# Kernel optimization log

Hardware: AMD Instinct MI355X
Metric: run time of the kernel (lower is better)

Reference implementation:

```python
import jax, jax.numpy as jnp
import numpy as np

N, E, P = 50000, 800000, 100000
IN, HID, H, L = 128, 128, 8, 3
D = HID // H


def setup_inputs() -> dict:
    key = jax.random.key(0)
    ks = jax.random.split(key, 24)
    rn = lambda k, shape, s: (jax.random.normal(k, shape, jnp.float32) * s)
    inp = {
        'x': jax.random.normal(ks[0], (N, IN), jnp.float32),
        'edge_src': jax.random.randint(ks[1], (E,), 0, N, jnp.int32),
        'edge_dst': jax.random.randint(ks[2], (E,), 0, N, jnp.int32),
        'edge_w': jax.random.uniform(ks[3], (E,), jnp.float32),
        'pos_src': jax.random.randint(ks[4], (P,), 0, N, jnp.int32),
        'pos_dst': jax.random.randint(ks[5], (P,), 0, N, jnp.int32),
        'neg_src': jax.random.randint(ks[6], (P,), 0, N, jnp.int32),
        'neg_dst': jax.random.randint(ks[7], (P,), 0, N, jnp.int32),
        # input projection
        'W_in': rn(ks[8], (IN, HID), IN ** -0.5),
        'b_in': jnp.zeros((HID,), jnp.float32),
        # per-layer HGT params (single ntype/etype -> plain matrices)
        'Wk': rn(ks[9], (L, HID, HID), HID ** -0.5),
        'Wq': rn(ks[10], (L, HID, HID), HID ** -0.5),
        'Wv': rn(ks[11], (L, HID, HID), HID ** -0.5),
        'att_w': rn(ks[12], (L, H, D, D), D ** -0.5),
        'msg_w': rn(ks[13], (L, H, D, D), D ** -0.5),
        'pri': jnp.ones((L, H), jnp.float32),
        'Wa': rn(ks[14], (L, HID, HID), HID ** -0.5),
        'skip': jnp.ones((L,), jnp.float32),
        # predictor MLP
        'W1': rn(ks[15], (HID, HID // 2), HID ** -0.5),
        'b1': jnp.zeros((HID // 2,), jnp.float32),
        'W2': rn(ks[16], (HID // 2, HID // 4), (HID // 2) ** -0.5),
        'b2': jnp.zeros((HID // 4,), jnp.float32),
        'W3': rn(ks[17], (HID // 4, 1), (HID // 4) ** -0.5),
        'b3': jnp.zeros((1,), jnp.float32),
    }
    return inp


def _hgt_forward(x, edge_src, edge_dst, edge_w, pos_src, pos_dst, neg_src, neg_dst,
                 W_in, b_in, Wk, Wq, Wv, att_w, msg_w, pri, Wa, skip,
                 W1, b1, W2, b2, W3, b3):
    n = x.shape[0]
    nheads = att_w.shape[1]
    d = att_w.shape[2]
    sqrt_d = jnp.asarray(d ** 0.5, x.dtype)
    h = jax.nn.relu(x @ W_in + b_in)
    nlayers = Wk.shape[0]
    for l in range(nlayers):
        k = (h @ Wk[l]).reshape(n, nheads, d)
        q = (h @ Wq[l]).reshape(n, nheads, d)
        v = (h @ Wv[l]).reshape(n, nheads, d)
        # relation-specific per-head transforms (etype constant -> node-level)
        kw = jnp.einsum('nhd,hde->nhe', k, att_w[l])
        mv = jnp.einsum('nhd,hde->nhe', v, msg_w[l])
        # per-edge attention logits [E, H]
        a = (kw[edge_src] * q[edge_dst]).sum(-1) * pri[l] / sqrt_d
        # edge softmax grouped by destination node
        amax = jax.ops.segment_max(a, edge_dst, num_segments=n)[edge_dst]
        ex = jnp.exp(a - amax)
        denom = jax.ops.segment_sum(ex, edge_dst, num_segments=n)[edge_dst]
        attn = ex / denom
        # weighted messages + scatter-sum  [E,H,D] -> [N,H,D]
        m = mv[edge_src] * edge_w[:, None, None] * attn[:, :, None]
        agg = jax.ops.segment_sum(m, edge_dst, num_segments=n).reshape(n, nheads * d)
        hn = agg @ Wa[l]  # linear_a (dropout is identity in eval)
        alpha = jax.nn.sigmoid(skip[l])
        h = hn * alpha + h * (1.0 - alpha)
        if l != nlayers - 1:
            h = jax.nn.relu(h)  # inter-layer relu (dropout identity)
    def predictor(z):
        z = jax.nn.leaky_relu(z @ W1 + b1, 0.2)
        z = jax.nn.leaky_relu(z @ W2 + b2, 0.2)
        return z @ W3 + b3
    h_pos = predictor(h[pos_src] * h[pos_dst])
    h_neg = predictor(h[neg_src] * h[neg_dst])
    return h_pos, h_neg, h


def reference(x, edge_src, edge_dst, edge_w, pos_src, pos_dst, neg_src, neg_dst,
              W_in, b_in, Wk, Wq, Wv, att_w, msg_w, pri, Wa, skip,
              W1, b1, W2, b2, W3, b3):
    return _hgt_forward(x, edge_src, edge_dst, edge_w, pos_src, pos_dst,
                        neg_src, neg_dst, W_in, b_in, Wk, Wq, Wv, att_w,
                        msg_w, pri, Wa, skip, W1, b1, W2, b2, W3, b3)
```

## Files before the change

kernel.cpp:

```cpp
#include <hip/hip_runtime.h>
#include <cstddef>

#define N_NODES 50000
#define N_EDGES 800000
#define N_PAIRS 100000

typedef float floatx4 __attribute__((ext_vector_type(4)));
typedef _Float16 half2v __attribute__((ext_vector_type(2)));
typedef _Float16 half4v __attribute__((ext_vector_type(4)));
typedef _Float16 half8v __attribute__((ext_vector_type(8)));

#define LWAIT { asm volatile("s_waitcnt lgkmcnt(0)" ::: "memory"); __builtin_amdgcn_sched_barrier(0); }

__device__ inline size_t packA(int m, int k, int K) {
  return ((size_t)((m >> 4) * (K >> 5) + (k >> 5)) << 9) +
         ((((unsigned)k >> 3) & 3) << 7) + ((m & 15) << 3) + (k & 7);
}

__device__ inline float fold_val(int l, int r, int j, const float* Wk, const float* Wq,
                                 const float* Wv, const float* att, const float* msg,
                                 const float* pri) {
  if (j >= 128 && j < 256) return Wq[(l * 128 + r) * 128 + (j - 128)];
  int jj = j & 127, hh = jj >> 4, e = jj & 15;
  const float* W = (j < 128) ? Wk : Wv;
  const float* T = (j < 128) ? att : msg;
  float s = 0.f;
#pragma unroll
  for (int d = 0; d < 16; d++)
    s += W[(l * 128 + r) * 128 + hh * 16 + d] * T[((l * 8 + hh) * 16 + d) * 16 + e];
  if (j < 128) s *= pri[l * 8 + hh] * 0.25f;
  return s;
}

__global__ void prep_fused(const float* __restrict__ W_in, const float* __restrict__ Wk,
                           const float* __restrict__ Wq, const float* __restrict__ Wv,
                           const float* __restrict__ att, const float* __restrict__ msg,
                           const float* __restrict__ pri, const float* __restrict__ Wa,
                           const float* __restrict__ W1, const float* __restrict__ W2,
                           _Float16* Wint, _Float16* Wcat, _Float16* Waf,
                           _Float16* W1f, _Float16* W2f,
                           const int* __restrict__ dst, int* __restrict__ deg, int E) {
  if (blockIdx.x >= 880) {
    int g = (blockIdx.x - 880) * 256 + threadIdx.x;
    if (g < E) atomicAdd(&deg[dst[g]], 1);
    return;
  }
  int gid = blockIdx.x * 256 + threadIdx.x;
  float v;
  _Float16* dt;
  size_t o;
  if (gid < 16384) {
    int n = gid >> 7, k = gid & 127;
    v = W_in[k * 128 + n];
    dt = Wint; o = packA(n, k, 128);
  } else if (gid < 163840) {
    int t = gid - 16384;
    int l = t / 49152, u = t - l * 49152;
    int n = u >> 7, k = u & 127;
    v = fold_val(l, k, n, Wk, Wq, Wv, att, msg, pri);
    dt = Wcat + (size_t)l * 49152;
    o = packA(n, k, 128);
  } else if (gid < 212992) {
    int t = gid - 163840;
    int l = t / 16384, u = t & 16383;
    int n = u >> 7, k = u & 127;
    v = Wa[(size_t)l * 16384 + k * 128 + n];
    dt = Waf + (size_t)l * 16384;
    o = packA(n, k, 128);
  } else if (gid < 221184) {
    int u = gid - 212992;
    int n = u >> 7, k = u & 127;
    v = W1[k * 64 + n];
    dt = W1f; o = packA(n, k, 128);
  } else if (gid < 225280) {
    int u = gid - 221184;
    int n = u >> 6, k = u & 63;
    v = (n < 32) ? W2[k * 32 + n] : 0.f;
    dt = W2f; o = packA(n, k, 64);
  } else {
    return;
  }
  dt[o] = (_Float16)v;
}

__global__ void scanA_kernel(const int* __restrict__ deg, int* __restrict__ offs,
                             int* __restrict__ bsum, int* __restrict__ bh, int n) {
  __shared__ int sm[256];
  __shared__ int lh[256];
  int t = threadIdx.x;
  int i = blockIdx.x * 256 + t;
  int dv = (i < n) ? deg[i] : 0;
  int v = (i < n) ? ((dv + 7) & ~7) : 0;
  sm[t] = v;
  __syncthreads();
  for (int off = 1; off < 256; off <<= 1) {
    int u = (t >= off) ? sm[t - off] : 0;
    __syncthreads();
    sm[t] += u;
    __syncthreads();
  }
  if (i < n) offs[i] = sm[t] - v;
  if (t == 255) bsum[blockIdx.x] = sm[255];
  lh[t] = 0;
  __syncthreads();
  if (i < n) atomicAdd(&lh[min(dv, 255)], 1);
  __syncthreads();
  if (lh[t]) atomicAdd(&bh[t], lh[t]);
}

__global__ void scanC_fused(int* __restrict__ offs, const int* __restrict__ bsum,
                            const int* __restrict__ bh, int* __restrict__ balloc,
                            const int* __restrict__ deg, int* __restrict__ cursor,
                            int* __restrict__ perm, int nb, int n) {
  __shared__ int sA[256], sB[256], bcurL[256], lh[256], lbase[256];
  int t = threadIdx.x;
  int i = blockIdx.x * 256 + t;
  int vA = (t < nb) ? bsum[t] : 0;
  sA[t] = vA;
  __syncthreads();
  for (int off = 1; off < 256; off <<= 1) {
    int u = (t >= off) ? sA[t - off] : 0;
    __syncthreads();
    sA[t] += u;
    __syncthreads();
  }
  int boffx = sA[blockIdx.x] - bsum[blockIdx.x];
  int vB = bh[255 - t];
  sB[t] = vB;
  __syncthreads();
  for (int off = 1; off < 256; off <<= 1) {
    int u = (t >= off) ? sB[t - off] : 0;
    __syncthreads();
    sB[t] += u;
    __syncthreads();
  }
  bcurL[255 - t] = sB[t] - vB;
  __syncthreads();
  int o = 0, dv = 0;
  if (i < n) {
    o = offs[i] + boffx;
    offs[i] = o;
    cursor[i] = o;
    dv = deg[i];
  }
  if (blockIdx.x == nb - 1 && t == nb - 1) offs[n] = sA[nb - 1];
  lh[t] = 0;
  __syncthreads();
  int b = 0, local = 0;
  if (i < n) {
    b = min(dv, 255);
    local = atomicAdd(&lh[b], 1);
  }
  __syncthreads();
  int cnt = lh[t];
  lbase[t] = cnt ? atomicAdd(&balloc[t], cnt) : 0;
  __syncthreads();
  if (i < n) perm[bcurL[b] + lbase[b] + local] = i;
}

__global__ void scatter_kernel(const int* __restrict__ src, const int* __restrict__ dst,
                               const float* __restrict__ w, int* __restrict__ cursor,
                               int2* __restrict__ eld, int E) {
  int g = blockIdx.x * blockDim.x + threadIdx.x;
  if (g < E) {
    int d = dst[g];
    int p = atomicAdd(&cursor[d], 1);
    eld[p] = make_int2(src[g], __float_as_int(w[g]));
  }
}

template <int FIRST>
__global__ __launch_bounds__(256) void fused_layer(
    const float* __restrict__ x, const _Float16* __restrict__ aggp,
    const _Float16* __restrict__ Wg1, const float* __restrict__ bias,
    const float* __restrict__ skipv, _Float16* __restrict__ hbuf,
    const _Float16* __restrict__ Wcat_l,
    _Float16* __restrict__ kwmv, _Float16* __restrict__ qbuf, int M) {
  int tid = threadIdx.x;
  int wave = tid >> 6, lane = tid & 63;
  int l16 = lane & 15, q = lane >> 4;
  int g = q, mloc = l16;
  int t0 = (blockIdx.x * 4 + wave) * 2;

  __shared__ _Float16 htile_s[4][2][2048];
  __shared__ float ldsT_s[4][16 * 68];
  float* myT = ldsT_s[wave];

  float alpha = 1.f, beta = 0.f;
  if (!FIRST) {
    float sv = *skipv;
    alpha = 1.f / (1.f + __expf(-sv));
    beta = 1.f - alpha;
  }

  floatx4 acc[2][8];
#pragma unroll
  for (int t = 0; t < 2; t++)
#pragma unroll
    for (int nt = 0; nt < 8; nt++) acc[t][nt] = (floatx4){0.f, 0.f, 0.f, 0.f};

#pragma unroll
  for (int kc = 0; kc < 4; kc++) {
    half8v a0, a1;
#pragma unroll
    for (int t = 0; t < 2; t++) {
      int tile = t0 + t;
      int tileC = (tile * 16 < M) ? tile : 0;
      half8v av;
      if (FIRST) {
        int row = min(tile * 16 + l16, M - 1);
        const float* p = x + (size_t)row * 128 + kc * 32 + q * 8;
        float4 u0 = *(const float4*)p, u1 = *(const float4*)(p + 4);
        float f[8] = {u0.x, u0.y, u0.z, u0.w, u1.x, u1.y, u1.z, u1.w};
#pragma unroll
        for (int i = 0; i < 8; i++) av[i] = (_Float16)f[i];
      } else {
        av = *(const half8v*)(aggp + (size_t)tileC * 2048 + (kc << 9) + lane * 8);
      }
      if (t == 0) a0 = av; else a1 = av;
    }
#pragma unroll
    for (int nt = 0; nt < 8; nt++) {
      half8v b = *(const half8v*)(Wg1 + (size_t)nt * 2048 + (kc << 9) + lane * 8);
      acc[0][nt] = __builtin_amdgcn_mfma_f32_16x16x32_f16(a0, b, acc[0][nt], 0, 0, 0);
      acc[1][nt] = __builtin_amdgcn_mfma_f32_16x16x32_f16(a1, b, acc[1][nt], 0, 0, 0);
    }
  }

#pragma unroll
  for (int t = 0; t < 2; t++) {
    int tile = t0 + t;
    bool alive = tile * 16 < M;
    int tileC = alive ? tile : 0;
#pragma unroll
    for (int p = 0; p < 2; p++) {
#pragma unroll
      for (int ntl = 0; ntl < 4; ntl++)
#pragma unroll
        for (int r = 0; r < 4; r++)
          myT[(q * 4 + r) * 68 + ntl * 16 + l16] = acc[t][p * 4 + ntl][r];
      LWAIT;
#pragma unroll
      for (int kc2 = 0; kc2 < 2; kc2++) {
        const float* rp = myT + mloc * 68 + kc2 * 32 + g * 8;
        floatx4 v0 = *(const floatx4*)rp;
        floatx4 v1 = *(const floatx4*)(rp + 4);
        float vals[8] = {v0[0], v0[1], v0[2], v0[3], v1[0], v1[1], v1[2], v1[3]};
        int col0 = p * 64 + kc2 * 32 + g * 8;
        size_t pbaseL = ((size_t)(tileC * 4 + (col0 >> 5)) << 9) + (size_t)lane * 8;
        if (FIRST) {
          float4 bb0 = *(const float4*)&bias[col0];
          float4 bb1 = *(const float4*)&bias[col0 + 4];
          float bbv[8] = {bb0.x, bb0.y, bb0.z, bb0.w, bb1.x, bb1.y, bb1.z, bb1.w};
#pragma unroll
          for (int j = 0; j < 8; j++) vals[j] = fmaxf(vals[j] + bbv[j], 0.f);
        } else {
          half8v hv = *(const half8v*)(hbuf + pbaseL);
#pragma unroll
          for (int j = 0; j < 8; j++)
            vals[j] = fmaxf(alpha * vals[j] + beta * (float)hv[j], 0.f);
        }
        half8v h8;
#pragma unroll
        for (int j = 0; j < 8; j++) h8[j] = (_Float16)vals[j];
        *(half8v*)(&htile_s[wave][t][0] + (((p * 2 + kc2) << 9) + (g << 7) + (mloc << 3))) = h8;
        if (alive) *(half8v*)(hbuf + pbaseL) = h8;
      }
      LWAIT;
    }
  }

  LWAIT;
  for (int c = 0; c < 6; c++) {
    floatx4 acc2[2][4];
#pragma unroll
    for (int t = 0; t < 2; t++)
#pragma unroll
      for (int nt = 0; nt < 4; nt++) acc2[t][nt] = (floatx4){0.f, 0.f, 0.f, 0.f};
#pragma unroll
    for (int kc = 0; kc < 4; kc++) {
      half8v af0 = *(const half8v*)(&htile_s[wave][0][0] + ((kc << 9) + lane * 8));
      half8v af1 = *(const half8v*)(&htile_s[wave][1][0] + ((kc << 9) + lane * 8));
#pragma unroll
      for (int nt = 0; nt < 4; nt++) {
        half8v b = *(const half8v*)(Wcat_l + (size_t)(c * 4 + nt) * 2048 + (kc << 9) + lane * 8);
        acc2[0][nt] = __builtin_amdgcn_mfma_f32_16x16x32_f16(af0, b, acc2[0][nt], 0, 0, 0);
        acc2[1][nt] = __builtin_amdgcn_mfma_f32_16x16x32_f16(af1, b, acc2[1][nt], 0, 0, 0);
      }
    }
#pragma unroll
    for (int t = 0; t < 2; t++) {
      int tile = t0 + t;
      bool alive = tile * 16 < M;
      int m0 = tile * 16;
#pragma unroll
      for (int ntl = 0; ntl < 4; ntl++)
#pragma unroll
        for (int r = 0; r < 4; r++)
          myT[(q * 4 + r) * 68 + ntl * 16 + l16] = acc2[t][ntl][r];
      LWAIT;
      if (alive) {
        int row = m0 + mloc;
#pragma unroll
        for (int kc2 = 0; kc2 < 2; kc2++) {
          const float* rp = myT + mloc * 68 + kc2 * 32 + g * 8;
          floatx4 v0 = *(const floatx4*)rp;
          floatx4 v1 = *(const floatx4*)(rp + 4);
          int col0 = c * 64 + kc2 * 32 + g * 8;
          int region = col0 >> 7;
          if (region == 1) {
            half8v h8;
#pragma unroll
            for (int j = 0; j < 4; j++) {
              h8[j] = (_Float16)v0[j];
              h8[j + 4] = (_Float16)v1[j];
            }
            *(half8v*)&qbuf[(size_t)row * 128 + (col0 - 128)] = h8;
          } else {
            int cc = col0 & 127;
            size_t base = (size_t)row * 256 + (size_t)(cc >> 2) * 8 + (region == 2 ? 4 : 0);
            half4v h0, h1;
#pragma unroll
            for (int j = 0; j < 4; j++) {
              h0[j] = (_Float16)v0[j];
              h1[j] = (_Float16)v1[j];
            }
            *(half4v*)&kwmv[base] = h0;
            *(half4v*)&kwmv[base + 8] = h1;
          }
        }
      }
      LWAIT;
    }
  }
}

__global__ __launch_bounds__(256) void gemm_last(
    const _Float16* __restrict__ aggp, const _Float16* __restrict__ Wg1,
    const float* __restrict__ skipv, const _Float16* __restrict__ hbuf,
    float* __restrict__ hfinal, _Float16* __restrict__ hrow, int M) {
  int tid = threadIdx.x;
  int wave = tid >> 6, lane = tid & 63;
  int l16 = lane & 15, q = lane >> 4;
  int g = q, mloc = l16;
  int t0 = (blockIdx.x * 4 + wave) * 2;

  __shared__ float ldsT_s[4][16 * 68];
  float* myT = ldsT_s[wave];

  float sv = *skipv;
  float alpha = 1.f / (1.f + __expf(-sv));
  float beta = 1.f - alpha;

  floatx4 acc[2][8];
#pragma unroll
  for (int t = 0; t < 2; t++)
#pragma unroll
    for (int nt = 0; nt < 8; nt++) acc[t][nt] = (floatx4){0.f, 0.f, 0.f, 0.f};

#pragma unroll
  for (int kc = 0; kc < 4; kc++) {
    int tC0 = (t0 * 16 < M) ? t0 : 0;
    int tC1 = ((t0 + 1) * 16 < M) ? (t0 + 1) : 0;
    half8v a0 = *(const half8v*)(aggp + (size_t)tC0 * 2048 + (kc << 9) + lane * 8);
    half8v a1 = *(const half8v*)(aggp + (size_t)tC1 * 2048 + (kc << 9) + lane * 8);
#pragma unroll
    for (int nt = 0; nt < 8; nt++) {
      half8v b = *(const half8v*)(Wg1 + (size_t)nt * 2048 + (kc << 9) + lane * 8);
      acc[0][nt] = __builtin_amdgcn_mfma_f32_16x16x32_f16(a0, b, acc[0][nt], 0, 0, 0);
      acc[1][nt] = __builtin_amdgcn_mfma_f32_16x16x32_f16(a1, b, acc[1][nt], 0, 0, 0);
    }
  }

#pragma unroll
  for (int t = 0; t < 2; t++) {
    int tile = t0 + t;
    bool alive = tile * 16 < M;
    int m0 = tile * 16;
#pragma unroll
    for (int p = 0; p < 2; p++) {
#pragma unroll
      for (int ntl = 0; ntl < 4; ntl++)
#pragma unroll
        for (int r = 0; r < 4; r++)
          myT[(q * 4 + r) * 68 + ntl * 16 + l16] = acc[t][p * 4 + ntl][r];
      LWAIT;
      if (alive) {
        int row = m0 + mloc;
#pragma unroll
        for (int kc2 = 0; kc2 < 2; kc2++) {
          const float* rp = myT + mloc * 68 + kc2 * 32 + g * 8;
          floatx4 v0 = *(const floatx4*)rp;
          floatx4 v1 = *(const floatx4*)(rp + 4);
          float vals[8] = {v0[0], v0[1], v0[2], v0[3], v1[0], v1[1], v1[2], v1[3]};
          int col0 = p * 64 + kc2 * 32 + g * 8;
          size_t pbase = ((size_t)(tile * 4 + (col0 >> 5)) << 9) + (size_t)lane * 8;
          half8v hv = *(const half8v*)(hbuf + pbase);
#pragma unroll
          for (int j = 0; j < 8; j++) vals[j] = alpha * vals[j] + beta * (float)hv[j];
          *(float4*)&hfinal[(size_t)row * 128 + col0] =
              make_float4(vals[0], vals[1], vals[2], vals[3]);
          *(float4*)&hfinal[(size_t)row * 128 + col0 + 4] =
              make_float4(vals[4], vals[5], vals[6], vals[7]);
          half8v h8;
#pragma unroll
          for (int j = 0; j < 8; j++) h8[j] = (_Float16)vals[j];
          *(half8v*)&hrow[(size_t)row * 128 + col0] = h8;
        }
      }
      LWAIT;
    }
  }
}

__global__ __launch_bounds__(256) void pred_fused(
    const _Float16* __restrict__ hrow,
    const int* __restrict__ ps, const int* __restrict__ pd,
    const int* __restrict__ ns, const int* __restrict__ nd,
    const _Float16* __restrict__ W1f, const float* __restrict__ b1,
    const _Float16* __restrict__ W2f, const float* __restrict__ b2,
    const float* __restrict__ W3, const float* __restrict__ b3,
    float* __restrict__ outd, int M) {
  int tid = threadIdx.x;
  int wave = tid >> 6, lane = tid & 63;
  int l16 = lane & 15, q = lane >> 4;
  int g = q, mloc = l16;
  int t0 = (blockIdx.x * 4 + wave) * 2;

  __shared__ _Float16 t1_s[4][2][1024];
  __shared__ float ldsT_s[4][16 * 68];
  float* myT = ldsT_s[wave];

  int pa[2], pb[2];
#pragma unroll
  for (int t = 0; t < 2; t++) {
    int gr = min((t0 + t) * 16 + l16, M - 1);
    bool pos = gr < N_PAIRS;
    int idx = pos ? gr : gr - N_PAIRS;
    pa[t] = pos ? ps[idx] : ns[idx];
    pb[t] = pos ? pd[idx] : nd[idx];
  }

  floatx4 acc1[2][4];
#pragma unroll
  for (int t = 0; t < 2; t++)
#pragma unroll
    for (int nt = 0; nt < 4; nt++) acc1[t][nt] = (floatx4){0.f, 0.f, 0.f, 0.f};

#pragma unroll
  for (int kc = 0; kc < 4; kc++) {
    int kbase = kc * 32 + q * 8;
    half8v a0, a1;
#pragma unroll
    for (int t = 0; t < 2; t++) {
      half8v ha = *(const half8v*)(hrow + (size_t)pa[t] * 128 + kbase);
      half8v hb = *(const half8v*)(hrow + (size_t)pb[t] * 128 + kbase);
      half8v av = ha * hb;
      if (t == 0) a0 = av; else a1 = av;
    }
#pragma unroll
    for (int nt = 0; nt < 4; nt++) {
      half8v b = *(const half8v*)(W1f + (size_t)nt * 2048 + (kc << 9) + lane * 8);
      acc1[0][nt] = __builtin_amdgcn_mfma_f32_16x16x32_f16(a0, b, acc1[0][nt], 0, 0, 0);
      acc1[1][nt] = __builtin_amdgcn_mfma_f32_16x16x32_f16(a1, b, acc1[1][nt], 0, 0, 0);
    }
  }

#pragma unroll
  for (int t = 0; t < 2; t++) {
#pragma unroll
    for (int ntl = 0; ntl < 4; ntl++)
#pragma unroll
      for (int r = 0; r < 4; r++)
        myT[(q * 4 + r) * 68 + ntl * 16 + l16] = acc1[t][ntl][r];
    LWAIT;
#pragma unroll
    for (int kc2 = 0; kc2 < 2; kc2++) {
      const float* rp = myT + mloc * 68 + kc2 * 32 + g * 8;
      floatx4 v0 = *(const floatx4*)rp;
      floatx4 v1 = *(const floatx4*)(rp + 4);
      float vals[8] = {v0[0], v0[1], v0[2], v0[3], v1[0], v1[1], v1[2], v1[3]};
      int col0 = kc2 * 32 + g * 8;
      float4 bb0 = *(const float4*)&b1[col0];
      float4 bb1 = *(const float4*)&b1[col0 + 4];
      float bbv[8] = {bb0.x, bb0.y, bb0.z, bb0.w, bb1.x, bb1.y, bb1.z, bb1.w};
      half8v h8;
#pragma unroll
      for (int j = 0; j < 8; j++) {
        float v = vals[j] + bbv[j];
        v = v > 0.f ? v : 0.2f * v;
        h8[j] = (_Float16)v;
      }
      *(half8v*)(&t1_s[wave][t][0] + ((kc2 << 9) + (g << 7) + (mloc << 3))) = h8;
    }
    LWAIT;
  }

  floatx4 acc2[2][2];
#pragma unroll
  for (int t = 0; t < 2; t++)
#pragma unroll
    for (int nt = 0; nt < 2; nt++) acc2[t][nt] = (floatx4){0.f, 0.f, 0.f, 0.f};
#pragma unroll
  for (int kc = 0; kc < 2; kc++) {
    half8v af0 = *(const half8v*)(&t1_s[wave][0][0] + ((kc << 9) + lane * 8));
    half8v af1 = *(const half8v*)(&t1_s[wave][1][0] + ((kc << 9) + lane * 8));
#pragma unroll
    for (int nt = 0; nt < 2; nt++) {
      half8v b = *(const half8v*)(W2f + (size_t)nt * 1024 + (kc << 9) + lane * 8);
      acc2[0][nt] = __builtin_amdgcn_mfma_f32_16x16x32_f16(af0, b, acc2[0][nt], 0, 0, 0);
      acc2[1][nt] = __builtin_amdgcn_mfma_f32_16x16x32_f16(af1, b, acc2[1][nt], 0, 0, 0);
    }
  }

  float bw[2], wv[2];
#pragma unroll
  for (int nt = 0; nt < 2; nt++) {
    int col = nt * 16 + l16;
    bw[nt] = b2[col];
    wv[nt] = W3[col];
  }
  float b3v = b3[0];
#pragma unroll
  for (int t = 0; t < 2; t++) {
    int m0 = (t0 + t) * 16;
    bool alive = m0 < M;
#pragma unroll
    for (int r = 0; r < 4; r++) {
      float partial = 0.f;
#pragma unroll
      for (int nt = 0; nt < 2; nt++) {
        float v = acc2[t][nt][r] + bw[nt];
        v = v > 0.f ? v : 0.2f * v;
        partial += v * wv[nt];
      }
      partial += __shfl_xor(partial, 1);
      partial += __shfl_xor(partial, 2);
      partial += __shfl_xor(partial, 4);
      partial += __shfl_xor(partial, 8);
      int row = m0 + q * 4 + r;
      if (l16 == 0 && alive && row < M) outd[row] = partial + b3v;
    }
  }
}

__global__ __launch_bounds__(256) void edge_agg_kernel(
    const _Float16* __restrict__ kwmv, const _Float16* __restrict__ qbuf,
    const int* __restrict__ poffs, const int2* __restrict__ eld,
    const int* __restrict__ perm,
    _Float16* __restrict__ agg, int n) {
  int hw = (blockIdx.x * 256 + threadIdx.x) >> 5;
  int stride = gridDim.x << 3;
  int c4 = threadIdx.x & 31;
  int ch = c4 << 2;
  for (int gw = hw; gw < n; gw += stride) {
    int node = perm[gw];
    half4v qv = *(const half4v*)&qbuf[(size_t)node * 128 + ch];
    half2v q01 = {qv[0], qv[1]}, q23 = {qv[2], qv[3]};
    float m = -1e30f, s = 0.f;
    float a0 = 0.f, a1 = 0.f, a2 = 0.f, a3 = 0.f;
    int beg = poffs[node], end = poffs[node + 1];
    if (beg < end) {
      int2 e0[8], e1[8], e2[8];
      half8v g0[8], g1[8];
#pragma unroll
      for (int i = 0; i < 8; i++) e0[i] = eld[beg + i];
#pragma unroll
      for (int i = 0; i < 8; i++)
        g0[i] = *(const half8v*)&kwmv[(size_t)max(e0[i].x, 0) * 256 + (size_t)c4 * 8];
#pragma unroll
      for (int i = 0; i < 8; i++) e1[i] = eld[beg + 8 + i];
      int j = beg;
      for (; j + 8 < end; j += 8) {
#pragma unroll
        for (int i = 0; i < 8; i++)
          g1[i] = *(const half8v*)&kwmv[(size_t)max(e1[i].x, 0) * 256 + (size_t)c4 * 8];
#pragma unroll
        for (int i = 0; i < 8; i++) e2[i] = eld[j + 16 + i];
        float p[8];
#pragma unroll
        for (int i = 0; i < 8; i++) {
          half2v k01 = {g0[i][0], g0[i][1]}, k23 = {g0[i][2], g0[i][3]};
          float d = __builtin_amdgcn_fdot2(
              k01, q01, __builtin_amdgcn_fdot2(k23, q23, 0.f, false), false);
          d += __shfl_xor(d, 1);
          d += __shfl_xor(d, 2);
          p[i] = (e0[i].x >= 0) ? d : -1e30f;
        }
        float nm = m;
#pragma unroll
        for (int i = 0; i < 8; i++) nm = fmaxf(nm, p[i]);
        float sc = __expf(m - nm);
        float t[8];
        float ssum = 0.f;
#pragma unroll
        for (int i = 0; i < 8; i++) {
          t[i] = __expf(p[i] - nm);
          ssum += t[i];
        }
        s = s * sc + ssum;
        a0 *= sc; a1 *= sc; a2 *= sc; a3 *= sc;
#pragma unroll
        for (int i = 0; i < 8; i++) {
          float w = (e0[i].x >= 0) ? __int_as_float(e0[i].y) : 0.f;
          float f = t[i] * w;
          a0 += f * (float)g0[i][4];
          a1 += f * (float)g0[i][5];
          a2 += f * (float)g0[i][6];
          a3 += f * (float)g0[i][7];
        }
        m = nm;
#pragma unroll
        for (int i = 0; i < 8; i++) {
          e0[i] = e1[i];
          e1[i] = e2[i];
          g0[i] = g1[i];
        }
      }
      {
        float p[8];
#pragma unroll
        for (int i = 0; i < 8; i++) {
          half2v k01 = {g0[i][0], g0[i][1]}, k23 = {g0[i][2], g0[i][3]};
          float d = __builtin_amdgcn_fdot2(
              k01, q01, __builtin_amdgcn_fdot2(k23, q23, 0.f, false), false);
          d += __shfl_xor(d, 1);
          d += __shfl_xor(d, 2);
          p[i] = (e0[i].x >= 0) ? d : -1e30f;
        }
        float nm = m;
#pragma unroll
        for (int i = 0; i < 8; i++) nm = fmaxf(nm, p[i]);
        float sc = __expf(m - nm);
        float t[8];
        float ssum = 0.f;
#pragma unroll
        for (int i = 0; i < 8; i++) {
          t[i] = __expf(p[i] - nm);
          ssum += t[i];
        }
        s = s * sc + ssum;
        a0 *= sc; a1 *= sc; a2 *= sc; a3 *= sc;
#pragma unroll
        for (int i = 0; i < 8; i++) {
          float w = (e0[i].x >= 0) ? __int_as_float(e0[i].y) : 0.f;
          float f = t[i] * w;
          a0 += f * (float)g0[i][4];
          a1 += f * (float)g0[i][5];
          a2 += f * (float)g0[i][6];
          a3 += f * (float)g0[i][7];
        }
      }
    }
    float inv = (s > 0.f) ? 1.f / s : 0.f;
    half4v out4;
    out4[0] = (_Float16)(a0 * inv);
    out4[1] = (_Float16)(a1 * inv);
    out4[2] = (_Float16)(a2 * inv);
    out4[3] = (_Float16)(a3 * inv);
    *(half4v*)&agg[packA(node, ch, 128)] = out4;
  }
}

extern "C" void kernel_launch(void* const* d_in, const int* in_sizes, int n_in,
                              void* d_out, int out_size, void* d_ws, size_t ws_size,
                              hipStream_t stream) {
  const float* x        = (const float*)d_in[0];
  const int*   edge_src = (const int*)d_in[1];
  const int*   edge_dst = (const int*)d_in[2];
  const float* edge_w   = (const float*)d_in[3];
  const int*   pos_src  = (const int*)d_in[4];
  const int*   pos_dst  = (const int*)d_in[5];
  const int*   neg_src  = (const int*)d_in[6];
  const int*   neg_dst  = (const int*)d_in[7];
  const float* W_in     = (const float*)d_in[8];
  const float* b_in     = (const float*)d_in[9];
  const float* Wk       = (const float*)d_in[10];
  const float* Wq       = (const float*)d_in[11];
  const float* Wv       = (const float*)d_in[12];
  const float* att_w    = (const float*)d_in[13];
  const float* msg_w    = (const float*)d_in[14];
  const float* pri      = (const float*)d_in[15];
  const float* Wa       = (const float*)d_in[16];
  const float* skip     = (const float*)d_in[17];
  const float* W1       = (const float*)d_in[18];
  const float* b1       = (const float*)d_in[19];
  const float* W2       = (const float*)d_in[20];
  const float* b2       = (const float*)d_in[21];
  const float* W3       = (const float*)d_in[22];
  const float* b3       = (const float*)d_in[23];
  float* out = (float*)d_out;

  char* W = (char*)d_ws;
  _Float16*  qbuf   = (_Float16*)(W + 0);
  _Float16*  kwmv   = (_Float16*)(W + 12800000);
  _Float16*  hbuf   = (_Float16*)(W + 38400000);
  _Float16*  agg    = (_Float16*)(W + 51200000);
  _Float16*  Wint   = (_Float16*)(W + 64000000);
  _Float16*  Wcat   = (_Float16*)(W + 64032768);
  _Float16*  Waf    = (_Float16*)(W + 64327680);
  _Float16*  W1f    = (_Float16*)(W + 64425984);
  _Float16*  W2f    = (_Float16*)(W + 64442368);
  int2*      eld    = (int2*)(W + 64450560);
  int*       deg    = (int*)(W + 77250560);
  int*       bh     = (int*)(W + 77450560);
  int*       balloc = (int*)(W + 77451584);
  int*       poffs  = (int*)(W + 77452608);
  int*       cursor = (int*)(W + 77652624);
  int*       perm   = (int*)(W + 77852624);
  int*       bsum   = (int*)(W + 78052624);
  _Float16*  hrow   = (_Float16*)(W + 78054912);
  float* hfinal = out + 2 * N_PAIRS;

  hipMemsetAsync(deg, 0, 202048, stream);
  hipMemsetAsync(eld, 0xFF, 9600000, stream);

  prep_fused<<<4005, 256, 0, stream>>>(W_in, Wk, Wq, Wv, att_w, msg_w, pri, Wa, W1, W2,
                                       Wint, Wcat, Waf, W1f, W2f,
                                       edge_dst, deg, N_EDGES);
  scanA_kernel<<<196, 256, 0, stream>>>(deg, poffs, bsum, bh, N_NODES);
  scanC_fused<<<196, 256, 0, stream>>>(poffs, bsum, bh, balloc, deg, cursor, perm,
                                       196, N_NODES);
  scatter_kernel<<<(N_EDGES + 255) / 256, 256, 0, stream>>>(
      edge_src, edge_dst, edge_w, cursor, eld, N_EDGES);

  fused_layer<1><<<391, 256, 0, stream>>>(x, nullptr, Wint, b_in, nullptr, hbuf,
                                          Wcat, kwmv, qbuf, N_NODES);
  edge_agg_kernel<<<2048, 256, 0, stream>>>(kwmv, qbuf, poffs, eld, perm, agg, N_NODES);
  fused_layer<0><<<391, 256, 0, stream>>>(nullptr, agg, Waf, nullptr, skip + 0, hbuf,
                                          Wcat + 49152, kwmv, qbuf, N_NODES);
  edge_agg_kernel<<<2048, 256, 0, stream>>>(kwmv, qbuf, poffs, eld, perm, agg, N_NODES);
  fused_layer<0><<<391, 256, 0, stream>>>(nullptr, agg, Waf + 16384, nullptr, skip + 1,
                                          hbuf, Wcat + 98304, kwmv, qbuf, N_NODES);
  edge_agg_kernel<<<2048, 256, 0, stream>>>(kwmv, qbuf, poffs, eld, perm, agg, N_NODES);
  gemm_last<<<391, 256, 0, stream>>>(agg, Waf + 32768, skip + 2, hbuf,
                                     hfinal, hrow, N_NODES);
  pred_fused<<<1563, 256, 0, stream>>>(hrow, pos_src, pos_dst, neg_src, neg_dst,
                                       W1f, b1, W2f, b2, W3, b3, out, 2 * N_PAIRS);
}
```

Baseline: 532.6 us.

## Two-pass bucketed edge scatter for locality; drop manual LDS wait barriers

Replaces the single random-atomic edge scatter with a two-pass approach. The first pass bins edges by destination block (256 nodes) using LDS counters and per-bucket global offsets computed from new per-block degree sums. The second pass then does the per-node cursor atomics and writes over a localized range, which is meant to improve cache locality of the atomics and the eld writes. The change also removes the explicit s_waitcnt/sched_barrier LWAIT macros in the GEMM kernels so the compiler can schedule LDS accesses freely. This risks correctness if the compiler does not insert the needed waits for cross-lane LDS transposes, and the extra pass adds memory traffic.

```diff
diff --git a/kernel.cpp b/kernel.cpp
--- a/kernel.cpp
+++ b/kernel.cpp
@@ -9,8 +9,6 @@
 typedef _Float16 half2v __attribute__((ext_vector_type(2)));
 typedef _Float16 half4v __attribute__((ext_vector_type(4)));
 typedef _Float16 half8v __attribute__((ext_vector_type(8)));
-
-#define LWAIT { asm volatile("s_waitcnt lgkmcnt(0)" ::: "memory"); __builtin_amdgcn_sched_barrier(0); }
 
 __device__ inline size_t packA(int m, int k, int K) {
   return ((size_t)((m >> 4) * (K >> 5) + (k >> 5)) << 9) +
@@ -84,13 +82,16 @@
 }
 
 __global__ void scanA_kernel(const int* __restrict__ deg, int* __restrict__ offs,
-                             int* __restrict__ bsum, int* __restrict__ bh, int n) {
+                             int* __restrict__ bsum, int* __restrict__ bh,
+                             int* __restrict__ bcnt, int n) {
   __shared__ int sm[256];
   __shared__ int lh[256];
+  __shared__ int dsum;
   int t = threadIdx.x;
   int i = blockIdx.x * 256 + t;
   int dv = (i < n) ? deg[i] : 0;
   int v = (i < n) ? ((dv + 7) & ~7) : 0;
+  if (t == 0) dsum = 0;
   sm[t] = v;
   __syncthreads();
   for (int off = 1; off < 256; off <<= 1) {
@@ -104,14 +105,17 @@
   lh[t] = 0;
   __syncthreads();
   if (i < n) atomicAdd(&lh[min(dv, 255)], 1);
+  atomicAdd(&dsum, dv);
   __syncthreads();
   if (lh[t]) atomicAdd(&bh[t], lh[t]);
+  if (t == 0) bcnt[blockIdx.x] = dsum;
 }
 
 __global__ void scanC_fused(int* __restrict__ offs, const int* __restrict__ bsum,
                             const int* __restrict__ bh, int* __restrict__ balloc,
                             const int* __restrict__ deg, int* __restrict__ cursor,
-                            int* __restrict__ perm, int nb, int n) {
+                            int* __restrict__ perm, const int* __restrict__ bcnt,
+                            int* __restrict__ bcur2, int nb, int n) {
   __shared__ int sA[256], sB[256], bcurL[256], lh[256], lbase[256];
   int t = threadIdx.x;
   int i = blockIdx.x * 256 + t;
@@ -156,16 +160,66 @@
   lbase[t] = cnt ? atomicAdd(&balloc[t], cnt) : 0;
   __syncthreads();
   if (i < n) perm[bcurL[b] + lbase[b] + local] = i;
-}
-
-__global__ void scatter_kernel(const int* __restrict__ src, const int* __restrict__ dst,
-                               const float* __restrict__ w, int* __restrict__ cursor,
-                               int2* __restrict__ eld, int E) {
+  if (blockIdx.x == 0) {
+    __shared__ int sC[256];
+    int vC = (t < nb) ? bcnt[t] : 0;
+    sC[t] = vC;
+    __syncthreads();
+    for (int off = 1; off < 256; off <<= 1) {
+      int u = (t >= off) ? sC[t - off] : 0;
+      __syncthreads();
+      sC[t] += u;
+      __syncthreads();
+    }
+    if (t < nb) bcur2[t] = sC[t] - vC;
+  }
+}
+
+__global__ __launch_bounds__(256) void scatterA_kernel(
+    const int* __restrict__ src, const int* __restrict__ dst,
+    const float* __restrict__ w, int* __restrict__ bcur2,
+    int2* __restrict__ ebuk_sw, int* __restrict__ ebuk_d, int E) {
+  __shared__ int lcnt[196], lbase[196];
+  int t = threadIdx.x;
+  for (int i = t; i < 196; i += 256) lcnt[i] = 0;
+  __syncthreads();
+  int g0 = blockIdx.x * 1024 + t;
+  int dv[4], sv[4], wv[4], lr[4], bk[4];
+#pragma unroll
+  for (int e = 0; e < 4; e++) {
+    int g = g0 + e * 256;
+    bk[e] = -1;
+    if (g < E) {
+      dv[e] = dst[g];
+      sv[e] = src[g];
+      wv[e] = __float_as_int(w[g]);
+      bk[e] = dv[e] >> 8;
+      lr[e] = atomicAdd(&lcnt[bk[e]], 1);
+    }
+  }
+  __syncthreads();
+  for (int i = t; i < 196; i += 256)
+    lbase[i] = lcnt[i] ? atomicAdd(&bcur2[i], lcnt[i]) : 0;
+  __syncthreads();
+#pragma unroll
+  for (int e = 0; e < 4; e++) {
+    if (bk[e] >= 0) {
+      int pos = lbase[bk[e]] + lr[e];
+      ebuk_d[pos] = dv[e];
+      ebuk_sw[pos] = make_int2(sv[e], wv[e]);
+    }
+  }
+}
+
+__global__ void scatterB_kernel(const int2* __restrict__ ebuk_sw,
+                                const int* __restrict__ ebuk_d,
+                                int* __restrict__ cursor, int2* __restrict__ eld,
+                                int E) {
   int g = blockIdx.x * blockDim.x + threadIdx.x;
   if (g < E) {
-    int d = dst[g];
+    int d = ebuk_d[g];
     int p = atomicAdd(&cursor[d], 1);
-    eld[p] = make_int2(src[g], __float_as_int(w[g]));
+    eld[p] = ebuk_sw[g];
   }
 }
 
@@ -239,7 +293,6 @@
 #pragma unroll
         for (int r = 0; r < 4; r++)
           myT[(q * 4 + r) * 68 + ntl * 16 + l16] = acc[t][p * 4 + ntl][r];
-      LWAIT;
 #pragma unroll
       for (int kc2 = 0; kc2 < 2; kc2++) {
         const float* rp = myT + mloc * 68 + kc2 * 32 + g * 8;
@@ -266,11 +319,9 @@
         *(half8v*)(&htile_s[wave][t][0] + (((p * 2 + kc2) << 9) + (g << 7) + (mloc << 3))) = h8;
         if (alive) *(half8v*)(hbuf + pbaseL) = h8;
       }
-      LWAIT;
-    }
-  }
-
-  LWAIT;
+    }
+  }
+
   for (int c = 0; c < 6; c++) {
     floatx4 acc2[2][4];
 #pragma unroll
@@ -298,7 +349,6 @@
 #pragma unroll
         for (int r = 0; r < 4; r++)
           myT[(q * 4 + r) * 68 + ntl * 16 + l16] = acc2[t][ntl][r];
-      LWAIT;
       if (alive) {
         int row = m0 + mloc;
 #pragma unroll
@@ -330,7 +380,6 @@
           }
         }
       }
-      LWAIT;
     }
   }
 }
@@ -384,7 +433,6 @@
 #pragma unroll
         for (int r = 0; r < 4; r++)
           myT[(q * 4 + r) * 68 + ntl * 16 + l16] = acc[t][p * 4 + ntl][r];
-      LWAIT;
       if (alive) {
         int row = m0 + mloc;
 #pragma unroll
@@ -408,7 +456,6 @@
           *(half8v*)&hrow[(size_t)row * 128 + col0] = h8;
         }
       }
-      LWAIT;
     }
   }
 }
@@ -473,7 +520,6 @@
 #pragma unroll
       for (int r = 0; r < 4; r++)
         myT[(q * 4 + r) * 68 + ntl * 16 + l16] = acc1[t][ntl][r];
-    LWAIT;
 #pragma unroll
     for (int kc2 = 0; kc2 < 2; kc2++) {
       const float* rp = myT + mloc * 68 + kc2 * 32 + g * 8;
@@ -493,7 +539,6 @@
       }
       *(half8v*)(&t1_s[wave][t][0] + ((kc2 << 9) + (g << 7) + (mloc << 3))) = h8;
     }
-    LWAIT;
   }
 
   floatx4 acc2[2][2];
@@ -709,8 +754,13 @@
   int*       cursor = (int*)(W + 77652624);
   int*       perm   = (int*)(W + 77852624);
   int*       bsum   = (int*)(W + 78052624);
-  _Float16*  hrow   = (_Float16*)(W + 78054912);
+  int*       bcnt   = (int*)(W + 78053648);
+  int*       bcur2  = (int*)(W + 78054672);
+  _Float16*  hrow   = (_Float16*)(W + 78055696);
   float* hfinal = out + 2 * N_PAIRS;
+
+  int2* ebuk_sw = (int2*)(W + 0);
+  int*  ebuk_d  = (int*)(W + 6400000);
 
   hipMemsetAsync(deg, 0, 202048, stream);
   hipMemsetAsync(eld, 0xFF, 9600000, stream);
@@ -718,11 +768,13 @@
   prep_fused<<<4005, 256, 0, stream>>>(W_in, Wk, Wq, Wv, att_w, msg_w, pri, Wa, W1, W2,
                                        Wint, Wcat, Waf, W1f, W2f,
                                        edge_dst, deg, N_EDGES);
-  scanA_kernel<<<196, 256, 0, stream>>>(deg, poffs, bsum, bh, N_NODES);
+  scanA_kernel<<<196, 256, 0, stream>>>(deg, poffs, bsum, bh, bcnt, N_NODES);
   scanC_fused<<<196, 256, 0, stream>>>(poffs, bsum, bh, balloc, deg, cursor, perm,
-                                       196, N_NODES);
-  scatter_kernel<<<(N_EDGES + 255) / 256, 256, 0, stream>>>(
-      edge_src, edge_dst, edge_w, cursor, eld, N_EDGES);
+                                       bcnt, bcur2, 196, N_NODES);
+  scatterA_kernel<<<782, 256, 0, stream>>>(edge_src, edge_dst, edge_w, bcur2,
+                                           ebuk_sw, ebuk_d, N_EDGES);
+  scatterB_kernel<<<(N_EDGES + 255) / 256, 256, 0, stream>>>(
+      ebuk_sw, ebuk_d, cursor, eld, N_EDGES);
 
   fused_layer<1><<<391, 256, 0, stream>>>(x, nullptr, Wint, b_in, nullptr, hbuf,
                                           Wcat, kwmv, qbuf, N_NODES);
```

New measurement: 542.0 us. About the same (+1.8%).
